# Kernel optimization log

Measured on AMD Instinct MI355X. Metric: run time of the kernel, lower is better.

## Reference

```python
import jax, jax.numpy as jnp
import numpy as np

# Dimensions (see shape_source)
U, B, D, H = 1024, 8, 512, 8
CHUNK = 32
NC = U // CHUNK          # 32 chunks
R, S, M = 32, 32, 32     # right-context rows, summary, memory
K = 31                   # depthwise conv kernel
Q = R + U + S            # 1088
KV = M + R + U           # 1088
NEG_INF = -1.0e8


def _build_attention_mask():
    """Chunk-wise Emformer mask: True = disallowed connection.
    Q layout: [R right-context rows | U utterance rows | S summary rows].
    KV layout: [M memory cols | R right-context cols | U utterance cols].
    Chunk c attends: memory banks < c, its own right-context col,
    its own chunk plus 1 left-context chunk of utterance."""
    mask = np.ones((Q, KV), dtype=bool)
    for c in range(NC):
        cols = np.zeros(KV, dtype=bool)
        cols[:min(c, M)] = True                    # memory of prior chunks
        cols[M + c] = True                         # this chunk's right context
        lo = max(0, c - 1) * CHUNK                 # 1 chunk of left context
        hi = (c + 1) * CHUNK
        cols[M + R + lo:M + R + hi] = True
        rows = [c] + list(range(R + c * CHUNK, R + (c + 1) * CHUNK)) + [R + U + c]
        mask[np.ix_(rows, np.nonzero(cols)[0])] = False
    return mask


def setup_inputs() -> dict:
    key = jax.random.key(0)
    ks = jax.random.split(key, 16)
    s = D ** -0.5
    inp = {
        'utterance': jax.random.normal(ks[0], (U, B, D), jnp.float32),
        'right_context': jax.random.normal(ks[1], (R, B, D), jnp.float32),
        'summary': jax.random.normal(ks[2], (S, B, D), jnp.float32),
        'memory': jax.random.normal(ks[3], (M, B, D), jnp.float32),
        'w_q': jax.random.normal(ks[4], (D, D), jnp.float32) * s,
        'b_q': jnp.zeros((D,), jnp.float32),
        'w_kv': jax.random.normal(ks[5], (2 * D, D), jnp.float32) * s,
        'b_kv': jnp.zeros((2 * D,), jnp.float32),
        'w_out': jax.random.normal(ks[6], (D, D), jnp.float32) * s,
        'b_out': jnp.zeros((D,), jnp.float32),
        'w_pw1': jax.random.normal(ks[7], (2 * D, D), jnp.float32) * s,
        'b_pw1': jnp.zeros((2 * D,), jnp.float32),
        'w_dw': jax.random.normal(ks[8], (D, 1, K), jnp.float32) * (K ** -0.5),
        'b_dw': jnp.zeros((D,), jnp.float32),
        'ln_g': jnp.ones((D,), jnp.float32),
        'ln_b': jnp.zeros((D,), jnp.float32),
        'w_pw2': jax.random.normal(ks[9], (D, D), jnp.float32) * s,
        'b_pw2': jnp.zeros((D,), jnp.float32),
        'lengths': jax.random.randint(ks[10], (B,), U // 2, U + 1, jnp.int32),
        'attention_mask': jnp.asarray(_build_attention_mask()),
    }
    return inp


def _conv_module(x, w_pw1, b_pw1, w_dw, b_dw, ln_g, ln_b, w_pw2, b_pw2):
    # x: (T, B, C) -> (B, C, T)
    x = x.transpose(1, 2, 0)
    x = jnp.einsum('bct,oc->bot', x, w_pw1) + b_pw1[:, None]
    a, g = jnp.split(x, 2, axis=1)
    x = a * jax.nn.sigmoid(g)                       # GLU over channel dim
    pad = (K - 1) // 2
    x = jax.lax.conv_general_dilated(
        x, w_dw, (1,), [(pad, pad)],
        dimension_numbers=('NCH', 'OIH', 'NCH'),
        feature_group_count=x.shape[1]) + b_dw[:, None]
    x = x.transpose(0, 2, 1)                        # (B, T, C) for LayerNorm
    mu = x.mean(-1, keepdims=True)
    var = ((x - mu) ** 2).mean(-1, keepdims=True)
    x = (x - mu) * jax.lax.rsqrt(var + 1e-5) * ln_g + ln_b
    x = x.transpose(0, 2, 1)
    x = x * jax.nn.sigmoid(x)                       # Swish
    x = jnp.einsum('bct,oc->bot', x, w_pw2) + b_pw2[:, None]
    return x.transpose(2, 0, 1)                     # (T, B, C)


def _emformer_forward(utterance, right_context, summary, memory,
                      w_q, b_q, w_kv, b_kv, w_out, b_out,
                      w_pw1, b_pw1, w_dw, b_dw, ln_g, ln_b, w_pw2, b_pw2,
                      lengths, attention_mask):
    d = D // H
    scaling = d ** -0.5
    q_in = jnp.concatenate([right_context, utterance, summary], axis=0)   # (Q,B,D)
    query = q_in @ w_q.T + b_q
    kv_in = jnp.concatenate([memory, right_context, utterance], axis=0)   # (KV,B,D)
    kv = kv_in @ w_kv.T + b_kv
    key_t, value_t = jnp.split(kv, 2, axis=2)

    def heads(t):  # (T,B,D) -> (B*H, T, d)
        return t.reshape(t.shape[0], B * H, d).transpose(1, 0, 2)

    qh, kh, vh = heads(query) * scaling, heads(key_t), heads(value_t)
    w = jnp.einsum('bqd,bkd->bqk', qh, kh)                                # (B*H,Q,KV)
    w = jnp.where(attention_mask[None], NEG_INF, w)
    # padding mask: pad positions are kv index >= KV - U + length
    pad = jnp.arange(KV)[None, :] >= (KV - U + lengths)[:, None]          # (B,KV)
    w = jnp.where(pad[:, None, :].repeat(H, axis=1).reshape(B * H, 1, KV), NEG_INF, w)
    p = jax.nn.softmax(w, axis=-1)
    attn = jnp.einsum('bqk,bkd->bqd', p, vh)                              # (B*H,Q,d)
    attn = attn.transpose(1, 0, 2).reshape(Q, B, D)
    outputs = attn @ w_out.T + b_out
    out_ru = outputs[:R + U]                                              # (R+U,B,D)
    # conformer convolution module with residual
    conv_out = _conv_module(out_ru, w_pw1, b_pw1, w_dw, b_dw,
                            ln_g, ln_b, w_pw2, b_pw2)
    return out_ru + conv_out


def reference(utterance, right_context, summary, memory,
              w_q, b_q, w_kv, b_kv, w_out, b_out,
              w_pw1, b_pw1, w_dw, b_dw, ln_g, ln_b, w_pw2, b_pw2,
              lengths, attention_mask):
    return _emformer_forward(utterance, right_context, summary, memory,
                             w_q, b_q, w_kv, b_kv, w_out, b_out,
                             w_pw1, b_pw1, w_dw, b_dw, ln_g, ln_b,
                             w_pw2, b_pw2, lengths, attention_mask)
```

## Files before the change

### kernel.cpp

```cpp
#include <hip/hip_runtime.h>
#include <hip/hip_bf16.h>
#include <math.h>

#define TQ    1056
#define TKV   1088

typedef __attribute__((ext_vector_type(8))) short short8;
typedef __attribute__((ext_vector_type(4))) short short4v;
typedef __attribute__((ext_vector_type(4))) float float4v;
typedef unsigned short ushort_t;

__device__ inline ushort_t f2bf(float x){
  union{float f; unsigned u;} v; v.f = x;
  unsigned r = v.u + 0x7fff + ((v.u >> 16) & 1);
  return (ushort_t)(r >> 16);
}
__device__ inline float bf2f(ushort_t h){
  union{unsigned u; float f;} v; v.u = ((unsigned)h) << 16;
  return v.f;
}

__device__ inline void gl_lds16(const ushort_t* g, ushort_t* l){
  __builtin_amdgcn_global_load_lds(
      (const __attribute__((address_space(1))) unsigned int*)g,
      (__attribute__((address_space(3))) unsigned int*)l, 16, 0, 0);
}

struct Cvt9 {
  const float* s[8];
  ushort_t*    d[8];
  const float* wdw;
  float*       wdwT;
  int bstart[9];
};

__global__ __launch_bounds__(256)
void cvt_f32_bf16(Cvt9 a)
{
  int blk = blockIdx.x;
  if (blk >= a.bstart[8]){
    int k = blk - a.bstart[8];
    int c = threadIdx.x;
    a.wdwT[k * 512 + c]       = a.wdw[c * 31 + k];
    a.wdwT[k * 512 + c + 256] = a.wdw[(c + 256) * 31 + k];
    return;
  }
  int seg = 0;
  while (blk >= a.bstart[seg + 1]) ++seg;
  int local = blk - a.bstart[seg];
  int idx = (local * 256 + threadIdx.x) * 4;
  float4v v = *(const float4v*)(a.s[seg] + idx);
  short4v o;
  #pragma unroll
  for (int j = 0; j < 4; ++j) ((ushort_t*)&o)[j] = f2bf(v[j]);
  *(short4v*)(a.d[seg] + idx) = o;
}

template<int MODE, int NX>
__global__ __launch_bounds__(256)
void gemm_bf16(const ushort_t* __restrict__ A, const ushort_t* __restrict__ Wb,
               const float* __restrict__ bias, const float* __restrict__ bias2,
               const ushort_t* __restrict__ residb,
               float* __restrict__ C0, ushort_t* __restrict__ U0,
               ushort_t* __restrict__ U1, int ny)
{
  const int blk = blockIdx.x;
  const int xcd = blk & 7;
  const int j   = blk >> 3;
  const int n_idx = j % NX;
  const int m_idx = (j / NX) * 8 + xcd;
  if (m_idx >= ny) return;

  __shared__ __align__(16) ushort_t As[128 * 32];
  __shared__ __align__(16) ushort_t Bs[128 * 32];
  const int tid  = threadIdx.x;
  const int w    = tid >> 6;
  const int lane = tid & 63;
  const int quad = lane >> 4;
  const int l16  = lane & 15;
  const int n0 = n_idx * 128;
  const int m0 = m_idx * 128;
  const int wm = (w >> 1) * 64;
  const int wn = (w & 1) * 64;
  const int srow = tid >> 2;
  const int sseg = (tid & 3) * 8;

  float4v acc[4][4];
  #pragma unroll
  for (int i = 0; i < 4; ++i)
    #pragma unroll
    for (int jj = 0; jj < 4; ++jj)
      acc[i][jj] = (float4v)(0.f);

  const ushort_t* Ag = A  + (size_t)(m0 + srow) * 512 + sseg;
  const ushort_t* Bg = Wb + (size_t)(n0 + srow) * 512 + sseg;
  ushort_t* la = &As[srow * 32 + sseg];
  ushort_t* lb = &Bs[srow * 32 + sseg];

  for (int kt = 0; kt < 16; ++kt){
    const int k0 = kt * 32;
    gl_lds16(Ag + k0,            la);
    gl_lds16(Ag + k0 + 64 * 512, la + 64 * 32);
    gl_lds16(Bg + k0,            lb);
    gl_lds16(Bg + k0 + 64 * 512, lb + 64 * 32);
    __syncthreads();
    short8 af[4], bf[4];
    #pragma unroll
    for (int i = 0; i < 4; ++i)
      af[i] = *(const short8*)&As[(wm + i*16 + l16) * 32 + quad * 8];
    #pragma unroll
    for (int jj = 0; jj < 4; ++jj)
      bf[jj] = *(const short8*)&Bs[(wn + jj*16 + l16) * 32 + quad * 8];
    #pragma unroll
    for (int i = 0; i < 4; ++i)
      #pragma unroll
      for (int jj = 0; jj < 4; ++jj)
        acc[i][jj] = __builtin_amdgcn_mfma_f32_16x16x32_bf16(
                        af[i], bf[jj], acc[i][jj], 0, 0, 0);
    __syncthreads();
  }

  #pragma unroll
  for (int jj = 0; jj < 4; ++jj){
    const int n = n0 + wn + jj*16 + l16;
    const float bn = (MODE == 4) ? (n < 512 ? bias[n] : bias2[n - 512])
                                 : bias[n];
    #pragma unroll
    for (int i = 0; i < 4; ++i){
      #pragma unroll
      for (int reg = 0; reg < 4; ++reg){
        const int m = m0 + wm + i*16 + quad*4 + reg;
        float v = acc[i][jj][reg] + bn;
        if (MODE == 4){
          if (n < 512){
            if (m >= 256){
              int mq = m - 256;
              int t = mq >> 3, b = mq & 7;
              int h = n >> 6, dh = n & 63;
              U0[(((size_t)(b*8 + h)) * TQ + t) * 64 + dh] = f2bf(v * 0.125f);
            }
          } else if (n < 1024){
            int n2 = n - 512;
            int t = m >> 3, b = m & 7;
            int h = n2 >> 6, dh = n2 & 63;
            C0 ? (void)0 : (void)0;
            ((ushort_t*)U1)[(((size_t)(b*8 + h)) * TKV + t) * 64 + dh] = f2bf(v);
          } else {
            int n2 = n - 1024;
            int t = m >> 3, b = m & 7;
            int h = n2 >> 6, dh = n2 & 63;
            ((ushort_t*)residb)[(((size_t)(b*8 + h)) * 64 + dh) * TKV + t] = f2bf(v);
          }
        } else if (MODE == 0){
          U0[(size_t)m * 512 + n] = f2bf(v);
        } else {
          v += bf2f(residb[(size_t)m * 512 + n]);
          C0[(size_t)m * 512 + n] = v;
        }
      }
    }
  }
}

__global__ __launch_bounds__(256)
void gemm_pw1_glu(const ushort_t* __restrict__ A, const ushort_t* __restrict__ Wb,
                  const float* __restrict__ bias, ushort_t* __restrict__ G, int ny)
{
  const int blk = blockIdx.x;
  const int xcd = blk & 7;
  const int j   = blk >> 3;
  const int n_idx = j % 4;
  const int m_idx = (j / 4) * 8 + xcd;
  if (m_idx >= ny) return;

  __shared__ __align__(16) ushort_t As [128 * 32];
  __shared__ __align__(16) ushort_t Bsa[128 * 32];
  __shared__ __align__(16) ushort_t Bsg[128 * 32];
  const int tid  = threadIdx.x;
  const int w    = tid >> 6;
  const int lane = tid & 63;
  const int quad = lane >> 4;
  const int l16  = lane & 15;
  const int n0 = n_idx * 128;
  const int m0 = m_idx * 128;
  const int wm = (w >> 1) * 64;
  const int wn = (w & 1) * 64;
  const int srow = tid >> 2;
  const int sseg = (tid & 3) * 8;

  float4v acca[4][4], accg[4][4];
  #pragma unroll
  for (int i = 0; i < 4; ++i)
    #pragma unroll
    for (int jj = 0; jj < 4; ++jj){
      acca[i][jj] = (float4v)(0.f);
      accg[i][jj] = (float4v)(0.f);
    }

  const ushort_t* Ag  = A  + (size_t)(m0 + srow) * 512 + sseg;
  const ushort_t* Bga = Wb + (size_t)(n0 + srow) * 512 + sseg;
  const ushort_t* Bgg = Wb + (size_t)(n0 + 512 + srow) * 512 + sseg;
  ushort_t* la  = &As [srow * 32 + sseg];
  ushort_t* lba = &Bsa[srow * 32 + sseg];
  ushort_t* lbg = &Bsg[srow * 32 + sseg];

  for (int kt = 0; kt < 16; ++kt){
    const int k0 = kt * 32;
    gl_lds16(Ag  + k0,            la);
    gl_lds16(Ag  + k0 + 64 * 512, la  + 64 * 32);
    gl_lds16(Bga + k0,            lba);
    gl_lds16(Bga + k0 + 64 * 512, lba + 64 * 32);
    gl_lds16(Bgg + k0,            lbg);
    gl_lds16(Bgg + k0 + 64 * 512, lbg + 64 * 32);
    __syncthreads();
    short8 af[4], ba[4], bg[4];
    #pragma unroll
    for (int i = 0; i < 4; ++i)
      af[i] = *(const short8*)&As[(wm + i*16 + l16) * 32 + quad * 8];
    #pragma unroll
    for (int jj = 0; jj < 4; ++jj){
      ba[jj] = *(const short8*)&Bsa[(wn + jj*16 + l16) * 32 + quad * 8];
      bg[jj] = *(const short8*)&Bsg[(wn + jj*16 + l16) * 32 + quad * 8];
    }
    #pragma unroll
    for (int i = 0; i < 4; ++i)
      #pragma unroll
      for (int jj = 0; jj < 4; ++jj){
        acca[i][jj] = __builtin_amdgcn_mfma_f32_16x16x32_bf16(
                         af[i], ba[jj], acca[i][jj], 0, 0, 0);
        accg[i][jj] = __builtin_amdgcn_mfma_f32_16x16x32_bf16(
                         af[i], bg[jj], accg[i][jj], 0, 0, 0);
      }
    __syncthreads();
  }

  #pragma unroll
  for (int jj = 0; jj < 4; ++jj){
    const int n = n0 + wn + jj*16 + l16;
    const float bna = bias[n];
    const float bng = bias[n + 512];
    #pragma unroll
    for (int i = 0; i < 4; ++i){
      #pragma unroll
      for (int reg = 0; reg < 4; ++reg){
        const int m = m0 + wm + i*16 + quad*4 + reg;
        float a = acca[i][jj][reg] + bna;
        float g = accg[i][jj][reg] + bng;
        G[(size_t)m * 512 + n] = f2bf(a * (1.f / (1.f + __expf(-g))));
      }
    }
  }
}

#define NPAD 72
#define VPAD 136

__global__ __launch_bounds__(256)
void attn_mfma(const ushort_t* __restrict__ qh, const ushort_t* __restrict__ kh,
               const ushort_t* __restrict__ vt, const int* __restrict__ lengths,
               ushort_t* __restrict__ attn_out)
{
  const int bh = blockIdx.x;
  const int c  = blockIdx.y;
  const int b  = bh >> 3, h = bh & 7;
  const int tid = threadIdx.x;
  const int w   = tid >> 6;
  const int lane = tid & 63;
  const int quad = lane >> 4;
  const int l16  = lane & 15;
  const int len  = lengths[b];

  __shared__ __align__(16) ushort_t Qs[48 * NPAD];
  __shared__ __align__(16) ushort_t KP[128 * NPAD];
  __shared__ __align__(16) ushort_t Vt[64 * VPAD];

  const int tb2 = 64 + (c > 0 ? c - 1 : 0) * 32;
  const int tb3 = 64 + c * 32;

  for (int e = tid; e < 384; e += 256){
    int row = e >> 3, sg = (e & 7) * 8;
    short8 v = {0,0,0,0,0,0,0,0};
    if (row == 0)
      v = *(const short8*)&qh[(((size_t)bh) * TQ + c) * 64 + sg];
    else if (row >= 16)
      v = *(const short8*)&qh[(((size_t)bh) * TQ + 32 + c*32 + (row-16)) * 64 + sg];
    *(short8*)&Qs[row * NPAD + sg] = v;
  }
  for (int e = tid; e < 1024; e += 256){
    int row = e >> 3, sg = (e & 7) * 8;
    int slot = row >> 5, jj = row & 31;
    int t = (slot == 0) ? jj : (slot == 1) ? 32 + jj : (slot == 2) ? tb2 + jj : tb3 + jj;
    *(short8*)&KP[row * NPAD + sg] =
        *(const short8*)&kh[(((size_t)bh) * TKV + t) * 64 + sg];
  }
  for (int e = tid; e < 1024; e += 256){
    int dh = e >> 4, sc = (e & 15) * 8;
    int slot = sc >> 5, jj = sc & 31;
    int t = (slot == 0) ? jj : (slot == 1) ? 32 + jj : (slot == 2) ? tb2 + jj : tb3 + jj;
    *(short8*)&Vt[dh * VPAD + sc] =
        *(const short8*)&vt[(((size_t)bh) * 64 + dh) * TKV + t];
  }
  __syncthreads();

  float4v Sf[3][2];
  #pragma unroll
  for (int mt = 0; mt < 3; ++mt)
    #pragma unroll
    for (int jt = 0; jt < 2; ++jt)
      Sf[mt][jt] = (float4v)(0.f);
  #pragma unroll
  for (int kc = 0; kc < 2; ++kc){
    short8 bfr[2];
    #pragma unroll
    for (int jt = 0; jt < 2; ++jt)
      bfr[jt] = *(const short8*)&KP[(w*32 + jt*16 + l16) * NPAD + kc*32 + quad*8];
    #pragma unroll
    for (int mt = 0; mt < 3; ++mt){
      short8 afr = *(const short8*)&Qs[(mt*16 + l16) * NPAD + kc*32 + quad*8];
      #pragma unroll
      for (int jt = 0; jt < 2; ++jt)
        Sf[mt][jt] = __builtin_amdgcn_mfma_f32_16x16x32_bf16(afr, bfr[jt], Sf[mt][jt], 0,0,0);
    }
  }

  bool live[2];
  #pragma unroll
  for (int jt = 0; jt < 2; ++jt){
    int jcol = jt*16 + l16;
    if      (w == 0) live[jt] = (jcol < c);
    else if (w == 1) live[jt] = (jcol == c);
    else if (w == 2) live[jt] = (c > 0) && ((c-1)*32 + jcol < len);
    else             live[jt] = (c*32 + jcol < len);
  }
  ushort_t pb[3][2][4];
  #pragma unroll
  for (int mt = 0; mt < 3; ++mt)
    #pragma unroll
    for (int jt = 0; jt < 2; ++jt)
      #pragma unroll
      for (int r = 0; r < 4; ++r)
        pb[mt][jt][r] = live[jt] ? f2bf(__expf(Sf[mt][jt][r])) : (ushort_t)0;

  __syncthreads();

  #pragma unroll
  for (int mt = 0; mt < 3; ++mt)
    #pragma unroll
    for (int r = 0; r < 4; ++r){
      int row = mt*16 + quad*4 + r;
      KP[row * VPAD + w*32 + l16]      = pb[mt][0][r];
      KP[row * VPAD + w*32 + 16 + l16] = pb[mt][1][r];
    }
  __syncthreads();

  const short8 ones = {0x3F80,0x3F80,0x3F80,0x3F80,0x3F80,0x3F80,0x3F80,0x3F80};
  float4v Of[3], Ls[3];
  #pragma unroll
  for (int mt = 0; mt < 3; ++mt){ Of[mt] = (float4v)(0.f); Ls[mt] = (float4v)(0.f); }
  #pragma unroll
  for (int kc = 0; kc < 4; ++kc){
    short8 bv = *(const short8*)&Vt[(w*16 + l16) * VPAD + kc*32 + quad*8];
    #pragma unroll
    for (int mt = 0; mt < 3; ++mt){
      short8 ap = *(const short8*)&KP[(mt*16 + l16) * VPAD + kc*32 + quad*8];
      Of[mt] = __builtin_amdgcn_mfma_f32_16x16x32_bf16(ap, bv,   Of[mt], 0,0,0);
      Ls[mt] = __builtin_amdgcn_mfma_f32_16x16x32_bf16(ap, ones, Ls[mt], 0,0,0);
    }
  }

  #pragma unroll
  for (int mt = 0; mt < 3; ++mt){
    #pragma unroll
    for (int r = 0; r < 4; ++r){
      int row = mt*16 + quad*4 + r;
      if (mt == 0 && row != 0) continue;
      float o = Of[mt][r] / Ls[mt][r];
      int t = (mt == 0) ? c : 32 + c*32 + (row - 16);
      attn_out[(((size_t)t) * 8 + b) * 512 + h*64 + w*16 + l16] = f2bf(o);
    }
  }
}

__global__ __launch_bounds__(512)
void conv_ln_silu3(const ushort_t* __restrict__ glub,
                   const float* __restrict__ w_dwT, const float* __restrict__ b_dw,
                   const float* __restrict__ ln_g, const float* __restrict__ ln_b,
                   ushort_t* __restrict__ zb)
{
  const int b  = blockIdx.y;
  const int t0 = blockIdx.x * 16;
  const int tid = threadIdx.x;
  __shared__ __align__(16) char smem[47104];
  ushort_t* in_t = (ushort_t*)smem;
  float*    S    = (float*)smem;

  for (int e = tid; e < 2944; e += 512){
    int row = e >> 6, sg = (e & 63) * 8;
    int tt = t0 - 15 + row;
    short8 v = {0,0,0,0,0,0,0,0};
    if (tt >= 0 && tt < TQ)
      v = *(const short8*)&glub[((size_t)tt * 8 + b) * 512 + sg];
    *(short8*)&in_t[row * 512 + sg] = v;
  }
  float wreg[31];
  #pragma unroll
  for (int k = 0; k < 31; ++k) wreg[k] = w_dwT[k * 512 + tid];
  const float bd = b_dw[tid];
  __syncthreads();

  float col[46];
  #pragma unroll 2
  for (int rr = 0; rr < 46; ++rr) col[rr] = bf2f(in_t[rr * 512 + tid]);

  float r[16];
  #pragma unroll
  for (int t = 0; t < 16; ++t){
    float acc = bd;
    #pragma unroll
    for (int k = 0; k < 31; ++k) acc += col[t + k] * wreg[k];
    r[t] = acc;
  }
  __syncthreads();
  #pragma unroll
  for (int t = 0; t < 16; ++t) S[t * 512 + tid] = r[t];
  __syncthreads();

  const int tg = tid >> 5;
  const int l  = tid & 31;
  float s = 0.f;
  #pragma unroll
  for (int i = 0; i < 16; ++i) s += S[tg * 512 + l + 32*i];
  #pragma unroll
  for (int off = 16; off >= 1; off >>= 1) s += __shfl_xor(s, off);
  const float mu = s * (1.f / 512.f);
  float s2 = 0.f;
  #pragma unroll
  for (int i = 0; i < 16; ++i){
    float d = S[tg * 512 + l + 32*i] - mu;
    s2 += d * d;
  }
  #pragma unroll
  for (int off = 16; off >= 1; off >>= 1) s2 += __shfl_xor(s2, off);
  const float rs = rsqrtf(s2 * (1.f / 512.f) + 1e-5f);

  const int c0 = l * 16;
  ushort_t ov[16];
  #pragma unroll
  for (int e = 0; e < 4; ++e){
    float4v xv = *(const float4v*)&S[tg * 512 + c0 + e*4];
    float4v gv = *(const float4v*)&ln_g[c0 + e*4];
    float4v bv = *(const float4v*)&ln_b[c0 + e*4];
    #pragma unroll
    for (int jj = 0; jj < 4; ++jj){
      float xn = (xv[jj] - mu) * rs * gv[jj] + bv[jj];
      ov[e*4 + jj] = f2bf(xn * (1.f / (1.f + __expf(-xn))));
    }
  }
  const size_t obase = ((size_t)(t0 + tg) * 8 + b) * 512 + c0;
  *(short8*)&zb[obase]     = *(short8*)&ov[0];
  *(short8*)&zb[obase + 8] = *(short8*)&ov[8];
}

extern "C" void kernel_launch(void* const* d_in, const int* in_sizes, int n_in,
                              void* d_out, int out_size, void* d_ws, size_t ws_size,
                              hipStream_t stream)
{
  (void)in_sizes; (void)n_in; (void)out_size; (void)ws_size;
  const float* utter = (const float*)d_in[0];
  const float* rctx  = (const float*)d_in[1];
  const float* memry = (const float*)d_in[3];
  const float* b_q   = (const float*)d_in[5];
  const float* b_kv  = (const float*)d_in[7];
  const float* b_out = (const float*)d_in[9];
  const float* b_pw1 = (const float*)d_in[11];
  const float* w_dw  = (const float*)d_in[12];
  const float* b_dw  = (const float*)d_in[13];
  const float* ln_g  = (const float*)d_in[14];
  const float* ln_b  = (const float*)d_in[15];
  const float* b_pw2 = (const float*)d_in[17];
  const int* lengths = (const int*)d_in[18];

  ushort_t* u = (ushort_t*)d_ws;
  ushort_t* memB  = u;
  ushort_t* rcB   = memB  + 131072;
  ushort_t* uttB  = rcB   + 131072;
  ushort_t* wqB   = uttB  + 4194304;
  ushort_t* wkvB  = wqB   + 262144;
  ushort_t* woutB = wkvB  + 524288;
  ushort_t* wpw1B = woutB + 262144;
  ushort_t* wpw2B = wpw1B + 524288;
  ushort_t* q_h   = wpw2B + 262144;
  ushort_t* k_h   = q_h   + 4325376;
  ushort_t* v_t   = k_h   + 4456448;
  ushort_t* attnb = v_t   + 4456448;
  ushort_t* outru_bf = attnb + 4325376;
  float*    wdwT  = (float*)(outru_bf + 4325376);
  ushort_t* glub  = q_h;
  ushort_t* zb    = attnb;
  float* outp = (float*)d_out;

  const ushort_t* A_kv = memB;

  Cvt9 ca;
  ca.s[0] = memry;                 ca.d[0] = memB;
  ca.s[1] = rctx;                  ca.d[1] = rcB;
  ca.s[2] = utter;                 ca.d[2] = uttB;
  ca.s[3] = (const float*)d_in[4]; ca.d[3] = wqB;
  ca.s[4] = (const float*)d_in[6]; ca.d[4] = wkvB;
  ca.s[5] = (const float*)d_in[8]; ca.d[5] = woutB;
  ca.s[6] = (const float*)d_in[10];ca.d[6] = wpw1B;
  ca.s[7] = (const float*)d_in[16];ca.d[7] = wpw2B;
  ca.wdw = w_dw; ca.wdwT = wdwT;
  int cnt[8] = {131072,131072,4194304,262144,524288,262144,524288,262144};
  int acc = 0;
  for (int i = 0; i < 8; ++i){ ca.bstart[i] = acc; acc += cnt[i] / 1024; }
  ca.bstart[8] = acc;
  cvt_f32_bf16<<<dim3(acc + 31), 256, 0, stream>>>(ca);

  gemm_bf16<4, 12><<<dim3(12 * 72), 256, 0, stream>>>(
      A_kv, wqB, b_q, b_kv, (const ushort_t*)v_t, nullptr, q_h, k_h, 68);
  attn_mfma<<<dim3(64, 32), 256, 0, stream>>>(q_h, k_h, v_t, lengths, attnb);
  gemm_bf16<0, 4><<<dim3(4 * 72), 256, 0, stream>>>(
      attnb, woutB, b_out, nullptr, nullptr, nullptr, outru_bf, nullptr, 66);
  gemm_pw1_glu<<<dim3(4 * 72), 256, 0, stream>>>(outru_bf, wpw1B, b_pw1, glub, 66);
  conv_ln_silu3<<<dim3(66, 8), 512, 0, stream>>>(glub, wdwT, b_dw, ln_g, ln_b, zb);
  gemm_bf16<3, 4><<<dim3(4 * 72), 256, 0, stream>>>(
      zb, wpw2B, b_pw2, nullptr, outru_bf, outp, nullptr, nullptr, 66);
}
```

Baseline: 285.9 us.

## Use BK=64 XOR-swizzled LDS tiles and narrower N tiles in GEMMs

The GEMM kernels now stage 64-wide K slices (8 iterations instead of 16), halving the number of barrier pairs. LDS reads use an XOR swizzle to avoid bank conflicts. The N tile is templated and shrunk to 64 for the 512-wide GEMMs (out, pw1-GLU, pw2), doubling the block count to about 576 for better CU occupancy on a 256-CU part. The trade-off is more LDS per block and reloading the A tile for every N tile.

```diff
diff --git a/kernel.cpp b/kernel.cpp
--- a/kernel.cpp
+++ b/kernel.cpp
@@ -56,7 +56,7 @@
   *(short4v*)(a.d[seg] + idx) = o;
 }
 
-template<int MODE, int NX>
+template<int MODE, int NX, int NT>
 __global__ __launch_bounds__(256)
 void gemm_bf16(const ushort_t* __restrict__ A, const ushort_t* __restrict__ Wb,
                const float* __restrict__ bias, const float* __restrict__ bias2,
@@ -64,6 +64,7 @@
                float* __restrict__ C0, ushort_t* __restrict__ U0,
                ushort_t* __restrict__ U1, int ny)
 {
+  constexpr int JN = NT / 32;
   const int blk = blockIdx.x;
   const int xcd = blk & 7;
   const int j   = blk >> 3;
@@ -71,57 +72,64 @@
   const int m_idx = (j / NX) * 8 + xcd;
   if (m_idx >= ny) return;
 
-  __shared__ __align__(16) ushort_t As[128 * 32];
-  __shared__ __align__(16) ushort_t Bs[128 * 32];
+  __shared__ __align__(16) ushort_t As[128 * 64];
+  __shared__ __align__(16) ushort_t Bs[NT * 64];
   const int tid  = threadIdx.x;
   const int w    = tid >> 6;
   const int lane = tid & 63;
   const int quad = lane >> 4;
   const int l16  = lane & 15;
-  const int n0 = n_idx * 128;
+  const int n0 = n_idx * NT;
   const int m0 = m_idx * 128;
   const int wm = (w >> 1) * 64;
-  const int wn = (w & 1) * 64;
-  const int srow = tid >> 2;
-  const int sseg = (tid & 3) * 8;
-
-  float4v acc[4][4];
+  const int wn = (w & 1) * (NT / 2);
+  const int srow = tid >> 3;
+  const int skseg = tid & 7;
+
+  float4v acc[4][JN];
   #pragma unroll
   for (int i = 0; i < 4; ++i)
     #pragma unroll
-    for (int jj = 0; jj < 4; ++jj)
+    for (int jj = 0; jj < JN; ++jj)
       acc[i][jj] = (float4v)(0.f);
 
-  const ushort_t* Ag = A  + (size_t)(m0 + srow) * 512 + sseg;
-  const ushort_t* Bg = Wb + (size_t)(n0 + srow) * 512 + sseg;
-  ushort_t* la = &As[srow * 32 + sseg];
-  ushort_t* lb = &Bs[srow * 32 + sseg];
-
-  for (int kt = 0; kt < 16; ++kt){
-    const int k0 = kt * 32;
-    gl_lds16(Ag + k0,            la);
-    gl_lds16(Ag + k0 + 64 * 512, la + 64 * 32);
-    gl_lds16(Bg + k0,            lb);
-    gl_lds16(Bg + k0 + 64 * 512, lb + 64 * 32);
+  for (int kt = 0; kt < 8; ++kt){
+    const int k0 = kt * 64;
+    #pragma unroll
+    for (int s = 0; s < 4; ++s){
+      int row = s*32 + srow;
+      gl_lds16(A + (size_t)(m0 + row) * 512 + k0 + ((skseg ^ (row & 7)) << 3),
+               &As[row * 64 + (skseg << 3)]);
+    }
+    #pragma unroll
+    for (int s = 0; s < NT/32; ++s){
+      int row = s*32 + srow;
+      gl_lds16(Wb + (size_t)(n0 + row) * 512 + k0 + ((skseg ^ (row & 7)) << 3),
+               &Bs[row * 64 + (skseg << 3)]);
+    }
     __syncthreads();
-    short8 af[4], bf[4];
-    #pragma unroll
-    for (int i = 0; i < 4; ++i)
-      af[i] = *(const short8*)&As[(wm + i*16 + l16) * 32 + quad * 8];
-    #pragma unroll
-    for (int jj = 0; jj < 4; ++jj)
-      bf[jj] = *(const short8*)&Bs[(wn + jj*16 + l16) * 32 + quad * 8];
-    #pragma unroll
-    for (int i = 0; i < 4; ++i)
-      #pragma unroll
-      for (int jj = 0; jj < 4; ++jj)
-        acc[i][jj] = __builtin_amdgcn_mfma_f32_16x16x32_bf16(
-                        af[i], bf[jj], acc[i][jj], 0, 0, 0);
+    #pragma unroll
+    for (int kc = 0; kc < 2; ++kc){
+      const int col = (((quad + (kc << 2)) ^ (l16 & 7)) << 3);
+      short8 af[4], bf[JN];
+      #pragma unroll
+      for (int i = 0; i < 4; ++i)
+        af[i] = *(const short8*)&As[(wm + i*16 + l16) * 64 + col];
+      #pragma unroll
+      for (int jj = 0; jj < JN; ++jj)
+        bf[jj] = *(const short8*)&Bs[(wn + jj*16 + l16) * 64 + col];
+      #pragma unroll
+      for (int i = 0; i < 4; ++i)
+        #pragma unroll
+        for (int jj = 0; jj < JN; ++jj)
+          acc[i][jj] = __builtin_amdgcn_mfma_f32_16x16x32_bf16(
+                          af[i], bf[jj], acc[i][jj], 0, 0, 0);
+    }
     __syncthreads();
   }
 
   #pragma unroll
-  for (int jj = 0; jj < 4; ++jj){
+  for (int jj = 0; jj < JN; ++jj){
     const int n = n0 + wn + jj*16 + l16;
     const float bn = (MODE == 4) ? (n < 512 ? bias[n] : bias2[n - 512])
                                  : bias[n];
@@ -143,8 +151,7 @@
             int n2 = n - 512;
             int t = m >> 3, b = m & 7;
             int h = n2 >> 6, dh = n2 & 63;
-            C0 ? (void)0 : (void)0;
-            ((ushort_t*)U1)[(((size_t)(b*8 + h)) * TKV + t) * 64 + dh] = f2bf(v);
+            U1[(((size_t)(b*8 + h)) * TKV + t) * 64 + dh] = f2bf(v);
           } else {
             int n2 = n - 1024;
             int t = m >> 3, b = m & 7;
@@ -169,73 +176,78 @@
   const int blk = blockIdx.x;
   const int xcd = blk & 7;
   const int j   = blk >> 3;
-  const int n_idx = j % 4;
-  const int m_idx = (j / 4) * 8 + xcd;
+  const int n_idx = j % 8;
+  const int m_idx = (j / 8) * 8 + xcd;
   if (m_idx >= ny) return;
 
-  __shared__ __align__(16) ushort_t As [128 * 32];
-  __shared__ __align__(16) ushort_t Bsa[128 * 32];
-  __shared__ __align__(16) ushort_t Bsg[128 * 32];
+  __shared__ __align__(16) ushort_t As [128 * 64];
+  __shared__ __align__(16) ushort_t Bsa[64 * 64];
+  __shared__ __align__(16) ushort_t Bsg[64 * 64];
   const int tid  = threadIdx.x;
   const int w    = tid >> 6;
   const int lane = tid & 63;
   const int quad = lane >> 4;
   const int l16  = lane & 15;
-  const int n0 = n_idx * 128;
+  const int n0 = n_idx * 64;
   const int m0 = m_idx * 128;
   const int wm = (w >> 1) * 64;
-  const int wn = (w & 1) * 64;
-  const int srow = tid >> 2;
-  const int sseg = (tid & 3) * 8;
-
-  float4v acca[4][4], accg[4][4];
+  const int wn = (w & 1) * 32;
+  const int srow = tid >> 3;
+  const int skseg = tid & 7;
+
+  float4v acca[4][2], accg[4][2];
   #pragma unroll
   for (int i = 0; i < 4; ++i)
     #pragma unroll
-    for (int jj = 0; jj < 4; ++jj){
+    for (int jj = 0; jj < 2; ++jj){
       acca[i][jj] = (float4v)(0.f);
       accg[i][jj] = (float4v)(0.f);
     }
 
-  const ushort_t* Ag  = A  + (size_t)(m0 + srow) * 512 + sseg;
-  const ushort_t* Bga = Wb + (size_t)(n0 + srow) * 512 + sseg;
-  const ushort_t* Bgg = Wb + (size_t)(n0 + 512 + srow) * 512 + sseg;
-  ushort_t* la  = &As [srow * 32 + sseg];
-  ushort_t* lba = &Bsa[srow * 32 + sseg];
-  ushort_t* lbg = &Bsg[srow * 32 + sseg];
-
-  for (int kt = 0; kt < 16; ++kt){
-    const int k0 = kt * 32;
-    gl_lds16(Ag  + k0,            la);
-    gl_lds16(Ag  + k0 + 64 * 512, la  + 64 * 32);
-    gl_lds16(Bga + k0,            lba);
-    gl_lds16(Bga + k0 + 64 * 512, lba + 64 * 32);
-    gl_lds16(Bgg + k0,            lbg);
-    gl_lds16(Bgg + k0 + 64 * 512, lbg + 64 * 32);
+  for (int kt = 0; kt < 8; ++kt){
+    const int k0 = kt * 64;
+    #pragma unroll
+    for (int s = 0; s < 4; ++s){
+      int row = s*32 + srow;
+      gl_lds16(A + (size_t)(m0 + row) * 512 + k0 + ((skseg ^ (row & 7)) << 3),
+               &As[row * 64 + (skseg << 3)]);
+    }
+    #pragma unroll
+    for (int s = 0; s < 2; ++s){
+      int row = s*32 + srow;
+      gl_lds16(Wb + (size_t)(n0 + row) * 512 + k0 + ((skseg ^ (row & 7)) << 3),
+               &Bsa[row * 64 + (skseg << 3)]);
+      gl_lds16(Wb + (size_t)(n0 + 512 + row) * 512 + k0 + ((skseg ^ (row & 7)) << 3),
+               &Bsg[row * 64 + (skseg << 3)]);
+    }
     __syncthreads();
-    short8 af[4], ba[4], bg[4];
-    #pragma unroll
-    for (int i = 0; i < 4; ++i)
-      af[i] = *(const short8*)&As[(wm + i*16 + l16) * 32 + quad * 8];
-    #pragma unroll
-    for (int jj = 0; jj < 4; ++jj){
-      ba[jj] = *(const short8*)&Bsa[(wn + jj*16 + l16) * 32 + quad * 8];
-      bg[jj] = *(const short8*)&Bsg[(wn + jj*16 + l16) * 32 + quad * 8];
-    }
-    #pragma unroll
-    for (int i = 0; i < 4; ++i)
-      #pragma unroll
-      for (int jj = 0; jj < 4; ++jj){
-        acca[i][jj] = __builtin_amdgcn_mfma_f32_16x16x32_bf16(
-                         af[i], ba[jj], acca[i][jj], 0, 0, 0);
-        accg[i][jj] = __builtin_amdgcn_mfma_f32_16x16x32_bf16(
-                         af[i], bg[jj], accg[i][jj], 0, 0, 0);
+    #pragma unroll
+    for (int kc = 0; kc < 2; ++kc){
+      const int col = (((quad + (kc << 2)) ^ (l16 & 7)) << 3);
+      short8 af[4], ba[2], bg[2];
+      #pragma unroll
+      for (int i = 0; i < 4; ++i)
+        af[i] = *(const short8*)&As[(wm + i*16 + l16) * 64 + col];
+      #pragma unroll
+      for (int jj = 0; jj < 2; ++jj){
+        ba[jj] = *(const short8*)&Bsa[(wn + jj*16 + l16) * 64 + col];
+        bg[jj] = *(const short8*)&Bsg[(wn + jj*16 + l16) * 64 + col];
       }
+      #pragma unroll
+      for (int i = 0; i < 4; ++i)
+        #pragma unroll
+        for (int jj = 0; jj < 2; ++jj){
+          acca[i][jj] = __builtin_amdgcn_mfma_f32_16x16x32_bf16(
+                           af[i], ba[jj], acca[i][jj], 0, 0, 0);
+          accg[i][jj] = __builtin_amdgcn_mfma_f32_16x16x32_bf16(
+                           af[i], bg[jj], accg[i][jj], 0, 0, 0);
+        }
+    }
     __syncthreads();
   }
 
   #pragma unroll
-  for (int jj = 0; jj < 4; ++jj){
+  for (int jj = 0; jj < 2; ++jj){
     const int n = n0 + wn + jj*16 + l16;
     const float bna = bias[n];
     const float bng = bias[n + 512];
@@ -517,13 +529,13 @@
   ca.bstart[8] = acc;
   cvt_f32_bf16<<<dim3(acc + 31), 256, 0, stream>>>(ca);
 
-  gemm_bf16<4, 12><<<dim3(12 * 72), 256, 0, stream>>>(
+  gemm_bf16<4, 12, 128><<<dim3(8 * 9 * 12), 256, 0, stream>>>(
       A_kv, wqB, b_q, b_kv, (const ushort_t*)v_t, nullptr, q_h, k_h, 68);
   attn_mfma<<<dim3(64, 32), 256, 0, stream>>>(q_h, k_h, v_t, lengths, attnb);
-  gemm_bf16<0, 4><<<dim3(4 * 72), 256, 0, stream>>>(
+  gemm_bf16<0, 8, 64><<<dim3(8 * 9 * 8), 256, 0, stream>>>(
       attnb, woutB, b_out, nullptr, nullptr, nullptr, outru_bf, nullptr, 66);
-  gemm_pw1_glu<<<dim3(4 * 72), 256, 0, stream>>>(outru_bf, wpw1B, b_pw1, glub, 66);
+  gemm_pw1_glu<<<dim3(8 * 9 * 8), 256, 0, stream>>>(outru_bf, wpw1B, b_pw1, glub, 66);
   conv_ln_silu3<<<dim3(66, 8), 512, 0, stream>>>(glub, wdwT, b_dw, ln_g, ln_b, zb);
-  gemm_bf16<3, 4><<<dim3(4 * 72), 256, 0, stream>>>(
+  gemm_bf16<3, 8, 64><<<dim3(8 * 9 * 8), 256, 0, stream>>>(
       zb, wpw2B, b_pw2, nullptr, outru_bf, outp, nullptr, nullptr, 66);
 }
```

Result: faster. 257.0 us (-10.1%).
